# Kernel optimization log

Measured on AMD Instinct MI355X. Metric: run time of the kernel, lower is better.

## Reference

```python
import jax, jax.numpy as jnp
import numpy as np

B, Q, C, N_PER, GS = 8, 2048, 256, 64, 8
H1, H2 = 256, 64
EPS = 1e-5


def make_grid():
    a = jnp.linspace(-0.1, 0.1, GS)
    gx, gy = jnp.meshgrid(a, a, indexing='ij')  # torch.meshgrid default 'ij'
    return jnp.stack([gx.reshape(-1), gy.reshape(-1)], axis=1)  # (n, 2)


def setup_inputs() -> dict:
    key = jax.random.key(0)
    ks = jax.random.split(key, 10)
    s = lambda k, shp, fan: jax.random.normal(k, shp, jnp.float32) / np.sqrt(fan)
    return {
        'tokens': jax.random.normal(ks[0], (B, Q, C), jnp.float32),
        'grid': make_grid(),
        'Wc': s(ks[1], (C, 3), C), 'bc': jnp.zeros((3,), jnp.float32),
        'W1': s(ks[2], (C + 2, H1), C + 2), 'b1': jnp.zeros((H1,), jnp.float32),
        'gamma1': jnp.ones((H1,), jnp.float32), 'beta1': jnp.zeros((H1,), jnp.float32),
        'W2': s(ks[3], (H1, H2), H1), 'b2': jnp.zeros((H2,), jnp.float32),
        'gamma2': jnp.ones((H2,), jnp.float32), 'beta2': jnp.zeros((H2,), jnp.float32),
        'W3': s(ks[4], (H2, 3), H2), 'b3': jnp.zeros((3,), jnp.float32),
    }


def batchnorm(x, gamma, beta):
    # BatchNorm1d in training mode: stats over batch (B*Q) and length (n) dims,
    # per channel (last axis here).
    mean = jnp.mean(x, axis=(0, 1, 2), keepdims=True)
    var = jnp.var(x, axis=(0, 1, 2), keepdims=True)
    return gamma * (x - mean) * jax.lax.rsqrt(var + EPS) + beta


def reference(tokens, grid, Wc, bc, W1, b1, gamma1, beta1, W2, b2, gamma2, beta2, W3, b3):
    coarse = tokens @ Wc + bc  # (B, Q, 3)
    # conv1 (1x1) on concat([tokens_expanded, grid]) == split matmul + broadcast add;
    # avoids materializing the (B,Q,n,C+2) concat explicitly.
    tok_part = tokens @ W1[:C]                 # (B, Q, H1)
    grid_part = grid @ W1[C:]                  # (n, H1)
    h = tok_part[:, :, None, :] + grid_part[None, None, :, :] + b1  # (B, Q, n, H1)
    h = jax.nn.relu(batchnorm(h, gamma1, beta1))
    h = jnp.einsum('bqnc,cd->bqnd', h, W2) + b2  # (B, Q, n, H2)
    h = jax.nn.relu(batchnorm(h, gamma2, beta2))
    disp = jnp.einsum('bqnc,cd->bqnd', h, W3) + b3  # (B, Q, n, 3)
    fine = (coarse[:, :, None, :] + disp).reshape(B, Q * N_PER, 3)
    return coarse, fine
```

## Files before the change

kernel.cpp:

```cpp
#include <hip/hip_runtime.h>
#include <hip/hip_bf16.h>

#define ROWS 16384
#define C_   256
#define H1_  256
#define H2_  64
#define EPSN 1e-5f

typedef __bf16 bf16x8 __attribute__((ext_vector_type(8)));
typedef __bf16 bf16x4 __attribute__((ext_vector_type(4)));
typedef __bf16 bf16x2 __attribute__((ext_vector_type(2)));
typedef float  f32x4  __attribute__((ext_vector_type(4)));
typedef float  f32x2  __attribute__((ext_vector_type(2)));

__device__ __forceinline__ bf16x2 cvt2(float a, float b) {
#if __has_builtin(__builtin_amdgcn_cvt_pk_bf16_f32)
    return __builtin_bit_cast(bf16x2, __builtin_amdgcn_cvt_pk_bf16_f32(a, b));
#else
    bf16x2 r; r[0] = (__bf16)a; r[1] = (__bf16)b; return r;
#endif
}

__global__ __launch_bounds__(256) void k0_pack(const float* __restrict__ W1,
                                               const float* __restrict__ W2,
                                               const float* __restrict__ W3,
                                               __bf16* __restrict__ W1p,
                                               __bf16* __restrict__ W2p,
                                               __bf16* __restrict__ W3p,
                                               float* __restrict__ zero_base) {
    int idx = blockIdx.x * 256 + threadIdx.x;
    if (idx < 65536) {
        int j = idx & 7, l = (idx >> 3) & 63, rest = idx >> 9;
        int ks = rest & 7, CT = rest >> 3;
        int k = ks * 32 + ((l >> 4) << 3) + j;
        int c = CT * 16 + (l & 15);
        W1p[idx] = (__bf16)W1[k * H1_ + c];
    } else {
        int i2 = idx - 65536;
        int j = i2 & 7, l = (i2 >> 3) & 63, rest = i2 >> 9;
        int ks = rest & 7, CK = rest >> 3;
        int k = ks * 32 + ((l >> 4) << 3) + j;
        int c2 = CK * 16 + (l & 15);
        W2p[i2] = (__bf16)W2[k * H2_ + c2];
    }
    if (idx < 1024) {
        int j = idx & 7, l = (idx >> 3) & 63, ks = idx >> 9;
        int k = ks * 32 + ((l >> 4) << 3) + j;
        int c = l & 15;
        W3p[idx] = (c < 3) ? (__bf16)W3[k * 3 + c] : (__bf16)0.f;
    }
    if (idx < 24576) zero_base[idx] = 0.0f;
}

__device__ __forceinline__ void prep_ctx(const float* __restrict__ grid,
                                         const float* __restrict__ W1,
                                         const float* __restrict__ a1p, int c0,
                                         f32x2* wgx2, f32x2* wgy2, float* A_) {
#pragma unroll
    for (int j = 0; j < 8; ++j) A_[j] = grid[2 * j + 1];
    f32x4 a0 = *(const f32x4*)(a1p + c0), a1h = *(const f32x4*)(a1p + c0 + 4);
    f32x4 x0 = *(const f32x4*)(W1 + C_ * H1_ + c0), x1 = *(const f32x4*)(W1 + C_ * H1_ + c0 + 4);
    f32x4 y0 = *(const f32x4*)(W1 + (C_ + 1) * H1_ + c0), yh = *(const f32x4*)(W1 + (C_ + 1) * H1_ + c0 + 4);
    float av[8] = {a0[0], a0[1], a0[2], a0[3], a1h[0], a1h[1], a1h[2], a1h[3]};
    float wx[8] = {x0[0], x0[1], x0[2], x0[3], x1[0], x1[1], x1[2], x1[3]};
    float wy[8] = {y0[0], y0[1], y0[2], y0[3], yh[0], yh[1], yh[2], yh[3]};
#pragma unroll
    for (int e = 0; e < 4; ++e) {
        wgx2[e][0] = av[2 * e] * wx[2 * e];     wgx2[e][1] = av[2 * e + 1] * wx[2 * e + 1];
        wgy2[e][0] = av[2 * e] * wy[2 * e];     wgy2[e][1] = av[2 * e + 1] * wy[2 * e + 1];
    }
}

__device__ __forceinline__ void stage16(__bf16* __restrict__ y1, int w, int c0, int nh,
                                        const float* __restrict__ a1p,
                                        const float* __restrict__ d1p,
                                        const f32x2* wgx2, const f32x2* wgy2,
                                        const float* A_, f32x4 t0, f32x4 t1) {
    f32x4 a0 = *(const f32x4*)(a1p + c0), a1h = *(const f32x4*)(a1p + c0 + 4);
    f32x4 d0 = *(const f32x4*)(d1p + c0), d1h = *(const f32x4*)(d1p + c0 + 4);
    int chunk = c0 >> 3;
    f32x2 base2[4];
    base2[0][0] = fmaf(a0[0], t0[0], d0[0]);  base2[0][1] = fmaf(a0[1], t0[1], d0[1]);
    base2[1][0] = fmaf(a0[2], t0[2], d0[2]);  base2[1][1] = fmaf(a0[3], t0[3], d0[3]);
    base2[2][0] = fmaf(a1h[0], t1[0], d1h[0]); base2[2][1] = fmaf(a1h[1], t1[1], d1h[1]);
    base2[3][0] = fmaf(a1h[2], t1[2], d1h[2]); base2[3][1] = fmaf(a1h[3], t1[3], d1h[3]);
#pragma unroll
    for (int ih = 0; ih < 2; ++ih) {
        float axs = A_[2 * w + ih];
        f32x2 ax2 = {axs, axs};
        f32x2 tc2[4];
#pragma unroll
        for (int e = 0; e < 4; ++e) tc2[e] = __builtin_elementwise_fma(wgx2[e], ax2, base2[e]);
#pragma unroll
        for (int kk = 0; kk < 4; ++kk) {
            int iy = nh + 2 * kk;
            float ays = A_[iy];
            f32x2 ay2 = {ays, ays};
            f32x2 z = {0.f, 0.f};
            int n = w * 16 + ih * 8 + iy;
            bf16x8 out;
            bf16x2* o2 = (bf16x2*)&out;
#pragma unroll
            for (int e = 0; e < 4; ++e) {
                f32x2 v = __builtin_elementwise_max(
                    __builtin_elementwise_fma(wgy2[e], ay2, tc2[e]), z);
                o2[e] = cvt2(v[0], v[1]);
            }
            *(bf16x8*)(&y1[n * 256 + ((chunk ^ iy) << 3)]) = out;
        }
    }
}

__global__ __launch_bounds__(256) void k1a(const float* __restrict__ tokens,
                                           const __bf16* __restrict__ W1p,
                                           const float* __restrict__ Wc,
                                           const float* __restrict__ bc,
                                           float* __restrict__ tokpart,
                                           float* __restrict__ coarse,
                                           float* __restrict__ p1s,
                                           float* __restrict__ p1q) {
    __shared__ __align__(16) __bf16 Al[16 * 264];
    int t = threadIdx.x, w = t >> 6, l = t & 63;
    int quad = l >> 4, col = l & 15;
    int rowbase = (blockIdx.x >> 1) * 16;
    int colhalf = blockIdx.x & 1;
    int slot = blockIdx.x & 31;

    bf16x8 bfr[16];
#pragma unroll
    for (int ctl = 0; ctl < 2; ++ctl)
#pragma unroll
        for (int ks = 0; ks < 8; ++ks) {
            int CT = colhalf * 8 + w * 2 + ctl;
            bfr[ctl * 8 + ks] = *(const bf16x8*)(W1p + (((CT * 8 + ks) * 64 + l) * 8));
        }
    {
        int r = t >> 4, cb = (t & 15) * 16;
        const float* src = tokens + (size_t)(rowbase + r) * C_ + cb;
        f32x4 t0 = *(const f32x4*)(src);
        f32x4 t1 = *(const f32x4*)(src + 4);
        f32x4 t2 = *(const f32x4*)(src + 8);
        f32x4 t3 = *(const f32x4*)(src + 12);
        bf16x8 v0, v1;
        bf16x2* p0 = (bf16x2*)&v0; bf16x2* p1 = (bf16x2*)&v1;
        p0[0] = cvt2(t0[0], t0[1]); p0[1] = cvt2(t0[2], t0[3]);
        p0[2] = cvt2(t1[0], t1[1]); p0[3] = cvt2(t1[2], t1[3]);
        p1[0] = cvt2(t2[0], t2[1]); p1[1] = cvt2(t2[2], t2[3]);
        p1[2] = cvt2(t3[0], t3[1]); p1[3] = cvt2(t3[2], t3[3]);
        *(bf16x8*)(&Al[r * 264 + cb]) = v0;
        *(bf16x8*)(&Al[r * 264 + cb + 8]) = v1;
    }
    __syncthreads();

    bf16x8 af[8];
#pragma unroll
    for (int ks = 0; ks < 8; ++ks)
        af[ks] = *(const bf16x8*)(&Al[col * 264 + ks * 32 + quad * 8]);

#pragma unroll
    for (int ctl = 0; ctl < 2; ++ctl) {
        f32x4 acc = {0.f, 0.f, 0.f, 0.f};
#pragma unroll
        for (int ks = 0; ks < 8; ++ks)
            acc = __builtin_amdgcn_mfma_f32_16x16x32_bf16(af[ks], bfr[ctl * 8 + ks], acc, 0, 0, 0);
        int c = colhalf * 128 + w * 32 + ctl * 16 + col;
        float s = 0.f, q = 0.f;
#pragma unroll
        for (int rr = 0; rr < 4; ++rr) {
            float v = acc[rr];
            tokpart[(size_t)(rowbase + quad * 4 + rr) * C_ + c] = v;
            s += v; q += v * v;
        }
        s += __shfl_xor(s, 16, 64); s += __shfl_xor(s, 32, 64);
        q += __shfl_xor(q, 16, 64); q += __shfl_xor(q, 32, 64);
        if (l < 16) {
            int cc = colhalf * 128 + w * 32 + ctl * 16 + l;
            atomicAdd(p1s + slot * C_ + cc, s);
            atomicAdd(p1q + slot * C_ + cc, q);
        }
    }
    if (colhalf == 0) {
        const f32x4* wcp = (const f32x4*)(Wc + l * 12);
        f32x4 wa = wcp[0], wb = wcp[1], wv = wcp[2];
        float wcl[12] = {wa[0], wa[1], wa[2], wa[3], wb[0], wb[1], wb[2], wb[3],
                         wv[0], wv[1], wv[2], wv[3]};
#pragma unroll
        for (int rr = 0; rr < 4; ++rr) {
            int r = w * 4 + rr;
            bf16x4 tv4 = *(const bf16x4*)(&Al[r * 264 + l * 4]);
            float p[3] = {0.f, 0.f, 0.f};
#pragma unroll
            for (int i = 0; i < 4; ++i) {
                float tvf = (float)tv4[i];
#pragma unroll
                for (int j = 0; j < 3; ++j) p[j] = fmaf(tvf, wcl[i * 3 + j], p[j]);
            }
#pragma unroll
            for (int off = 1; off < 64; off <<= 1)
#pragma unroll
                for (int j = 0; j < 3; ++j) p[j] += __shfl_xor(p[j], off, 64);
            if (l == 0) {
#pragma unroll
                for (int j = 0; j < 3; ++j)
                    coarse[(size_t)(rowbase + r) * 3 + j] = p[j] + bc[j];
            }
        }
    }
}

__global__ void k1b(const float* __restrict__ grid, const float* __restrict__ W1,
                    const float* __restrict__ gamma1, const float* __restrict__ beta1,
                    const float* __restrict__ p1s, const float* __restrict__ p1q,
                    float* __restrict__ a1o, float* __restrict__ d1o) {
    int t = threadIdx.x;
    float S = 0.f, Qq = 0.f;
    for (int s = 0; s < 32; ++s) { S += p1s[s * C_ + t]; Qq += p1q[s * C_ + t]; }
    float mean_t = S / (float)ROWS;
    float var_t = Qq / (float)ROWS - mean_t * mean_t;
    float wx = W1[C_ * H1_ + t];
    float wy = W1[(C_ + 1) * H1_ + t];
    float mg = 0.f, qg = 0.f;
    for (int n = 0; n < 64; ++n) {
        float gv = grid[2 * n] * wx + grid[2 * n + 1] * wy;
        mg += gv; qg += gv * gv;
    }
    mg *= (1.f / 64.f);
    float var_g = qg * (1.f / 64.f) - mg * mg;
    float a1 = gamma1[t] * rsqrtf(var_t + var_g + EPSN);
    a1o[t] = a1;
    d1o[t] = beta1[t] - a1 * (mean_t + mg);
}

template <bool SPILL>
__global__ __launch_bounds__(256) void k2(const float* __restrict__ tokpart,
                                          const float* __restrict__ grid,
                                          const float* __restrict__ W1,
                                          const __bf16* __restrict__ W2p,
                                          const float* __restrict__ a1,
                                          const float* __restrict__ d1,
                                          float* __restrict__ p2s,
                                          float* __restrict__ p2q,
                                          __bf16* __restrict__ h2s) {
    __shared__ __align__(16) __bf16 y1[64 * 256];
    int t = threadIdx.x, w = t >> 6, l = t & 63;
    int quad = l >> 4, col = l & 15;
    int wn = w >> 1, wc = w & 1;
    int c0 = (l & 31) * 8, nh = l >> 5;
    int sw = col & 7;

    bf16x8 bfr[16];
#pragma unroll
    for (int ck = 0; ck < 2; ++ck)
#pragma unroll
        for (int ks = 0; ks < 8; ++ks)
            bfr[ck * 8 + ks] = *(const bf16x8*)(W2p + ((((wc * 2 + ck) * 8 + ks) * 64 + l) * 8));

    f32x2 wgx2[4], wgy2[4]; float A_[8];
    prep_ctx(grid, W1, a1, c0, wgx2, wgy2, A_);

    float s[2][4] = {}, q[2][4] = {};

    const float* tokbase = tokpart + (size_t)blockIdx.x * 8 * C_;
    f32x4 t0 = *(const f32x4*)(tokbase + c0);
    f32x4 t1 = *(const f32x4*)(tokbase + c0 + 4);

#pragma unroll 1
    for (int r8 = 0; r8 < 8; ++r8) {
        int row = blockIdx.x * 8 + r8;
        int nr = (r8 < 7) ? (r8 + 1) : 7;
        f32x4 n0 = *(const f32x4*)(tokbase + (size_t)nr * C_ + c0);
        f32x4 n1 = *(const f32x4*)(tokbase + (size_t)nr * C_ + c0 + 4);

        stage16(y1, w, c0, nh, a1, d1, wgx2, wgy2, A_, t0, t1);
        __syncthreads();
#pragma unroll
        for (int rt = 0; rt < 2; ++rt) {
            int rowb = (wn * 32 + rt * 16 + col) * 256;
            bf16x8 af[8];
#pragma unroll
            for (int ks = 0; ks < 8; ++ks)
                af[ks] = *(const bf16x8*)(&y1[rowb + (((ks * 4 + quad) ^ sw) << 3)]);
#pragma unroll
            for (int ck = 0; ck < 2; ++ck) {
                f32x4 acc = {0.f, 0.f, 0.f, 0.f};
#pragma unroll
                for (int ks = 0; ks < 8; ++ks)
                    acc = __builtin_amdgcn_mfma_f32_16x16x32_bf16(bfr[ck * 8 + ks], af[ks], acc, 0, 0, 0);
#pragma unroll
                for (int rr = 0; rr < 4; ++rr) {
                    s[ck][rr] += acc[rr];
                    q[ck][rr] += acc[rr] * acc[rr];
                }
                if constexpr (SPILL) {
                    bf16x4 v; bf16x2* v2 = (bf16x2*)&v;
                    v2[0] = cvt2(acc[0], acc[1]);
                    v2[1] = cvt2(acc[2], acc[3]);
                    *(bf16x4*)(h2s + (size_t)row * 4096 +
                               ((w * 2 + rt) * 2 + ck) * 256 + l * 4) = v;
                }
            }
        }
        __syncthreads();
        t0 = n0; t1 = n1;
    }
    int slot = ((blockIdx.x << 1) | wn) & 63;
#pragma unroll
    for (int ck = 0; ck < 2; ++ck)
#pragma unroll
        for (int rr = 0; rr < 4; ++rr) {
            float sv = s[ck][rr], qv = q[ck][rr];
            sv += __shfl_xor(sv, 1, 64); sv += __shfl_xor(sv, 2, 64);
            sv += __shfl_xor(sv, 4, 64); sv += __shfl_xor(sv, 8, 64);
            qv += __shfl_xor(qv, 1, 64); qv += __shfl_xor(qv, 2, 64);
            qv += __shfl_xor(qv, 4, 64); qv += __shfl_xor(qv, 8, 64);
            if (col == 0) {
                int c2 = wc * 32 + ck * 16 + quad * 4 + rr;
                atomicAdd(p2s + slot * H2_ + c2, sv);
                atomicAdd(p2q + slot * H2_ + c2, qv);
            }
        }
}

__global__ void k2b(const float* __restrict__ p2s, const float* __restrict__ p2q,
                    const float* __restrict__ gamma2, const float* __restrict__ beta2,
                    float* __restrict__ a2o, float* __restrict__ d2o) {
    int t = threadIdx.x;
    float S = 0.f, Qq = 0.f;
    for (int s = 0; s < 64; ++s) { S += p2s[s * H2_ + t]; Qq += p2q[s * H2_ + t]; }
    const float invN = 1.f / ((float)ROWS * 64.f);
    float mean = S * invN;
    float var = Qq * invN - mean * mean;
    float a2 = gamma2[t] * rsqrtf(var + EPSN);
    a2o[t] = a2;
    d2o[t] = beta2[t] - a2 * mean;
}

__global__ __launch_bounds__(256) void k3s(const __bf16* __restrict__ h2s,
                                           const float* __restrict__ a2,
                                           const float* __restrict__ d2p,
                                           const __bf16* __restrict__ W3p,
                                           const float* __restrict__ b3,
                                           const float* __restrict__ coarse,
                                           float* __restrict__ fine) {
    __shared__ __align__(16) __bf16 y2l[8][64 * 64];
    __shared__ __align__(16) float finebuf[8 * 192];
    int t = threadIdx.x, w = t >> 6, l = t & 63;
    int quad = l >> 4, col = l & 15;
    int wn = w >> 1, wc = w & 1;
    int sw = col & 7;

    bf16x8 wfr[2];
#pragma unroll
    for (int ks = 0; ks < 2; ++ks)
        wfr[ks] = *(const bf16x8*)(W3p + ((ks * 64 + l) * 8));

    float a2v[8], d2v[8];
#pragma unroll
    for (int ck = 0; ck < 2; ++ck)
#pragma unroll
        for (int rr = 0; rr < 4; ++rr) {
            int c2 = wc * 32 + ck * 16 + quad * 4 + rr;
            a2v[ck * 4 + rr] = a2[c2];
            d2v[ck * 4 + rr] = d2p[c2];
        }

#pragma unroll 1
    for (int r8 = 0; r8 < 8; ++r8) {
        size_t row = (size_t)blockIdx.x * 8 + r8;
        const __bf16* src = h2s + row * 4096 + l * 4;
        bf16x4 u[2][2];
#pragma unroll
        for (int rt = 0; rt < 2; ++rt)
#pragma unroll
            for (int ck = 0; ck < 2; ++ck)
                u[rt][ck] = *(const bf16x4*)(src + ((w * 2 + rt) * 2 + ck) * 256);
#pragma unroll
        for (int rt = 0; rt < 2; ++rt) {
            int n = wn * 32 + rt * 16 + col;
#pragma unroll
            for (int ck = 0; ck < 2; ++ck) {
                float y0 = fmaxf(fmaf(a2v[ck * 4 + 0], (float)u[rt][ck][0], d2v[ck * 4 + 0]), 0.f);
                float y1v = fmaxf(fmaf(a2v[ck * 4 + 1], (float)u[rt][ck][1], d2v[ck * 4 + 1]), 0.f);
                float y2 = fmaxf(fmaf(a2v[ck * 4 + 2], (float)u[rt][ck][2], d2v[ck * 4 + 2]), 0.f);
                float y3 = fmaxf(fmaf(a2v[ck * 4 + 3], (float)u[rt][ck][3], d2v[ck * 4 + 3]), 0.f);
                bf16x4 v; bf16x2* v2 = (bf16x2*)&v;
                v2[0] = cvt2(y0, y1v); v2[1] = cvt2(y2, y3);
                int chunk = wc * 4 + ck * 2 + (quad >> 1);
                *(bf16x4*)(&y2l[r8][n * 64 + ((chunk ^ sw) << 3) + (quad & 1) * 4]) = v;
            }
        }
    }
    __syncthreads();
    float b3v = (col < 3) ? b3[col] : 0.f;
#pragma unroll 1
    for (int r8 = 0; r8 < 8; ++r8) {
        int row = blockIdx.x * 8 + r8;
        int rowb = (w * 16 + col) * 64;
        bf16x8 af2[2];
#pragma unroll
        for (int ks = 0; ks < 2; ++ks)
            af2[ks] = *(const bf16x8*)(&y2l[r8][rowb + (((ks * 4 + quad) ^ sw) << 3)]);
        f32x4 acc = {0.f, 0.f, 0.f, 0.f};
        acc = __builtin_amdgcn_mfma_f32_16x16x32_bf16(af2[0], wfr[0], acc, 0, 0, 0);
        acc = __builtin_amdgcn_mfma_f32_16x16x32_bf16(af2[1], wfr[1], acc, 0, 0, 0);
        if (col < 3) {
            float cj = coarse[row * 3 + col] + b3v;
#pragma unroll
            for (int rr = 0; rr < 4; ++rr)
                finebuf[r8 * 192 + (w * 16 + quad * 4 + rr) * 3 + col] = acc[rr] + cj;
        }
    }
    __syncthreads();
    {
        float* dst = fine + (size_t)blockIdx.x * 1536;
        const f32x4* fb = (const f32x4*)finebuf;
        *(f32x4*)(dst + 4 * t) = fb[t];
        if (t < 128) *(f32x4*)(dst + 1024 + 4 * t) = fb[256 + t];
    }
}

__global__ __launch_bounds__(256) void k3r(const float* __restrict__ tokpart,
                                           const float* __restrict__ grid,
                                           const float* __restrict__ W1,
                                           const __bf16* __restrict__ W2p,
                                           const float* __restrict__ a1,
                                           const float* __restrict__ d1,
                                           const __bf16* __restrict__ W3p,
                                           const float* __restrict__ a2,
                                           const float* __restrict__ d2p,
                                           const float* __restrict__ b3,
                                           const float* __restrict__ coarse,
                                           float* __restrict__ fine) {
    __shared__ __align__(16) __bf16 y1[64 * 256];
    __shared__ __align__(16) __bf16 y2l[64 * 72];
    __shared__ __align__(16) float finebuf[8 * 192];
    int t = threadIdx.x, w = t >> 6, l = t & 63;
    int quad = l >> 4, col = l & 15;
    int wn = w >> 1, wc = w & 1;
    int c0 = (l & 31) * 8, nh = l >> 5;
    int sw = col & 7;

    bf16x8 bfr[16];
#pragma unroll
    for (int ck = 0; ck < 2; ++ck)
#pragma unroll
        for (int ks = 0; ks < 8; ++ks)
            bfr[ck * 8 + ks] = *(const bf16x8*)(W2p + ((((wc * 2 + ck) * 8 + ks) * 64 + l) * 8));
    bf16x8 wfr[2];
#pragma unroll
    for (int ks = 0; ks < 2; ++ks)
        wfr[ks] = *(const bf16x8*)(W3p + ((ks * 64 + l) * 8));

    f32x2 wgx2[4], wgy2[4]; float A_[8];
    prep_ctx(grid, W1, a1, c0, wgx2, wgy2, A_);

    float a2v[8], d2v[8];
#pragma unroll
    for (int ck = 0; ck < 2; ++ck)
#pragma unroll
        for (int rr = 0; rr < 4; ++rr) {
            int c2 = wc * 32 + ck * 16 + quad * 4 + rr;
            a2v[ck * 4 + rr] = a2[c2];
            d2v[ck * 4 + rr] = d2p[c2];
        }
    float b3v = (col < 3) ? b3[col] : 0.f;

#pragma unroll 1
    for (int r8 = 0; r8 < 8; ++r8) {
        int row = blockIdx.x * 8 + r8;
        const float* tokrow = tokpart + (size_t)row * C_;
        f32x4 t0 = *(const f32x4*)(tokrow + c0);
        f32x4 t1 = *(const f32x4*)(tokrow + c0 + 4);
        stage16(y1, w, c0, nh, a1, d1, wgx2, wgy2, A_, t0, t1);
        __syncthreads();
#pragma unroll
        for (int rt = 0; rt < 2; ++rt) {
            int rowb = (wn * 32 + rt * 16 + col) * 256;
            bf16x8 af[8];
#pragma unroll
            for (int ks = 0; ks < 8; ++ks)
                af[ks] = *(const bf16x8*)(&y1[rowb + (((ks * 4 + quad) ^ sw) << 3)]);
#pragma unroll
            for (int ck = 0; ck < 2; ++ck) {
                f32x4 acc = {0.f, 0.f, 0.f, 0.f};
#pragma unroll
                for (int ks = 0; ks < 8; ++ks)
                    acc = __builtin_amdgcn_mfma_f32_16x16x32_bf16(bfr[ck * 8 + ks], af[ks], acc, 0, 0, 0);
                bf16x4 v; bf16x2* v2 = (bf16x2*)&v;
                float y0 = fmaxf(fmaf(a2v[ck * 4 + 0], acc[0], d2v[ck * 4 + 0]), 0.f);
                float y1v = fmaxf(fmaf(a2v[ck * 4 + 1], acc[1], d2v[ck * 4 + 1]), 0.f);
                float y2 = fmaxf(fmaf(a2v[ck * 4 + 2], acc[2], d2v[ck * 4 + 2]), 0.f);
                float y3 = fmaxf(fmaf(a2v[ck * 4 + 3], acc[3], d2v[ck * 4 + 3]), 0.f);
                v2[0] = cvt2(y0, y1v); v2[1] = cvt2(y2, y3);
                *(bf16x4*)(&y2l[(wn * 32 + rt * 16 + col) * 72 + wc * 32 + ck * 16 + quad * 4]) = v;
            }
        }
        __syncthreads();
        bf16x8 af2[2];
#pragma unroll
        for (int ks = 0; ks < 2; ++ks)
            af2[ks] = *(const bf16x8*)(&y2l[(w * 16 + col) * 72 + ks * 32 + quad * 8]);
        f32x4 d2acc = {0.f, 0.f, 0.f, 0.f};
        d2acc = __builtin_amdgcn_mfma_f32_16x16x32_bf16(af2[0], wfr[0], d2acc, 0, 0, 0);
        d2acc = __builtin_amdgcn_mfma_f32_16x16x32_bf16(af2[1], wfr[1], d2acc, 0, 0, 0);
        if (col < 3) {
            float cj = coarse[row * 3 + col] + b3v;
#pragma unroll
            for (int rr = 0; rr < 4; ++rr)
                finebuf[r8 * 192 + (w * 16 + quad * 4 + rr) * 3 + col] = d2acc[rr] + cj;
        }
        __syncthreads();
    }
    {
        float* dst = fine + (size_t)blockIdx.x * 1536;
        const f32x4* fb = (const f32x4*)finebuf;
        *(f32x4*)(dst + 4 * t) = fb[t];
        if (t < 128) *(f32x4*)(dst + 1024 + 4 * t) = fb[256 + t];
    }
}

extern "C" void kernel_launch(void* const* d_in, const int* in_sizes, int n_in,
                              void* d_out, int out_size, void* d_ws, size_t ws_size,
                              hipStream_t stream) {
    (void)in_sizes; (void)n_in; (void)out_size;
    const float* tokens = (const float*)d_in[0];
    const float* grid   = (const float*)d_in[1];
    const float* Wc     = (const float*)d_in[2];
    const float* bc     = (const float*)d_in[3];
    const float* W1     = (const float*)d_in[4];
    const float* gamma1 = (const float*)d_in[6];
    const float* beta1  = (const float*)d_in[7];
    const float* W2     = (const float*)d_in[8];
    const float* gamma2 = (const float*)d_in[10];
    const float* beta2  = (const float*)d_in[11];
    const float* W3     = (const float*)d_in[12];
    const float* b3     = (const float*)d_in[13];

    char* ws = (char*)d_ws;
    __bf16* W1p     = (__bf16*)(ws);
    __bf16* W2p     = (__bf16*)(ws + 131072);
    float*  p1s     = (float*)(ws + 163840);
    float*  p1q     = (float*)(ws + 196608);
    float*  p2s     = (float*)(ws + 229376);
    float*  p2q     = (float*)(ws + 245760);
    float*  a1      = (float*)(ws + 262144);
    float*  d1      = (float*)(ws + 263168);
    float*  a2      = (float*)(ws + 264192);
    float*  d2p     = (float*)(ws + 264448);
    __bf16* W3p     = (__bf16*)(ws + 264704);
    float*  tokpart = (float*)(ws + 266752);
    __bf16* h2s     = (__bf16*)(ws + 17043968);

    const size_t SPILL_NEED = 17043968ull + 134217728ull;
    bool spill = ws_size >= SPILL_NEED;

    float* coarse = (float*)d_out;
    float* fine   = (float*)d_out + (size_t)ROWS * 3;

    k0_pack<<<320, 256, 0, stream>>>(W1, W2, W3, W1p, W2p, W3p, p1s);
    k1a<<<2048, 256, 0, stream>>>(tokens, W1p, Wc, bc, tokpart, coarse, p1s, p1q);
    k1b<<<1, 256, 0, stream>>>(grid, W1, gamma1, beta1, p1s, p1q, a1, d1);
    if (spill) {
        k2<true><<<ROWS / 8, 256, 0, stream>>>(tokpart, grid, W1, W2p, a1, d1, p2s, p2q, h2s);
        k2b<<<1, 64, 0, stream>>>(p2s, p2q, gamma2, beta2, a2, d2p);
        k3s<<<ROWS / 8, 256, 0, stream>>>(h2s, a2, d2p, W3p, b3, coarse, fine);
    } else {
        k2<false><<<ROWS / 8, 256, 0, stream>>>(tokpart, grid, W1, W2p, a1, d1, p2s, p2q, h2s);
        k2b<<<1, 64, 0, stream>>>(p2s, p2q, gamma2, beta2, a2, d2p);
        k3r<<<ROWS / 8, 256, 0, stream>>>(tokpart, grid, W1, W2p, a1, d1, W3p, a2, d2p, b3, coarse, fine);
    }
}
```

Before: 203.5 us.

## Make each wave own whole row tiles to drop block barriers in k2 and k3s

In k2, each wave now computes all 64 output channels for its own 16 grid points instead of splitting points and channels across wave pairs. Each wave only reads the LDS rows it staged itself, so both per-iteration __syncthreads are removed. k3s follows the same per-wave ownership with a small wave-private LDS buffer, fusing its load/normalize pass with the MFMA pass and dropping the block barrier between them. The trade-off is twice as many W2 fragments held in registers (launch bounds now request 2 blocks per CU), which raises register pressure, and correctness now depends on stage16 writing only rows its own wave consumes.

```diff
diff --git a/kernel.cpp b/kernel.cpp
--- a/kernel.cpp
+++ b/kernel.cpp
@@ -232,33 +232,32 @@
 }
 
 template <bool SPILL>
-__global__ __launch_bounds__(256) void k2(const float* __restrict__ tokpart,
-                                          const float* __restrict__ grid,
-                                          const float* __restrict__ W1,
-                                          const __bf16* __restrict__ W2p,
-                                          const float* __restrict__ a1,
-                                          const float* __restrict__ d1,
-                                          float* __restrict__ p2s,
-                                          float* __restrict__ p2q,
-                                          __bf16* __restrict__ h2s) {
+__global__ __launch_bounds__(256, 2) void k2(const float* __restrict__ tokpart,
+                                             const float* __restrict__ grid,
+                                             const float* __restrict__ W1,
+                                             const __bf16* __restrict__ W2p,
+                                             const float* __restrict__ a1,
+                                             const float* __restrict__ d1,
+                                             float* __restrict__ p2s,
+                                             float* __restrict__ p2q,
+                                             __bf16* __restrict__ h2s) {
     __shared__ __align__(16) __bf16 y1[64 * 256];
     int t = threadIdx.x, w = t >> 6, l = t & 63;
     int quad = l >> 4, col = l & 15;
-    int wn = w >> 1, wc = w & 1;
     int c0 = (l & 31) * 8, nh = l >> 5;
     int sw = col & 7;
 
-    bf16x8 bfr[16];
-#pragma unroll
-    for (int ck = 0; ck < 2; ++ck)
+    bf16x8 bfr[32];
+#pragma unroll
+    for (int ck = 0; ck < 4; ++ck)
 #pragma unroll
         for (int ks = 0; ks < 8; ++ks)
-            bfr[ck * 8 + ks] = *(const bf16x8*)(W2p + ((((wc * 2 + ck) * 8 + ks) * 64 + l) * 8));
+            bfr[ck * 8 + ks] = *(const bf16x8*)(W2p + (((ck * 8 + ks) * 64 + l) * 8));
 
     f32x2 wgx2[4], wgy2[4]; float A_[8];
     prep_ctx(grid, W1, a1, c0, wgx2, wgy2, A_);
 
-    float s[2][4] = {}, q[2][4] = {};
+    float s[4][4] = {}, q[4][4] = {};
 
     const float* tokbase = tokpart + (size_t)blockIdx.x * 8 * C_;
     f32x4 t0 = *(const f32x4*)(tokbase + c0);
@@ -272,40 +271,34 @@
         f32x4 n1 = *(const f32x4*)(tokbase + (size_t)nr * C_ + c0 + 4);
 
         stage16(y1, w, c0, nh, a1, d1, wgx2, wgy2, A_, t0, t1);
-        __syncthreads();
-#pragma unroll
-        for (int rt = 0; rt < 2; ++rt) {
-            int rowb = (wn * 32 + rt * 16 + col) * 256;
-            bf16x8 af[8];
+        int rowb = (w * 16 + col) * 256;
+        bf16x8 af[8];
+#pragma unroll
+        for (int ks = 0; ks < 8; ++ks)
+            af[ks] = *(const bf16x8*)(&y1[rowb + (((ks * 4 + quad) ^ sw) << 3)]);
+#pragma unroll
+        for (int ck = 0; ck < 4; ++ck) {
+            f32x4 acc = {0.f, 0.f, 0.f, 0.f};
 #pragma unroll
             for (int ks = 0; ks < 8; ++ks)
-                af[ks] = *(const bf16x8*)(&y1[rowb + (((ks * 4 + quad) ^ sw) << 3)]);
-#pragma unroll
-            for (int ck = 0; ck < 2; ++ck) {
-                f32x4 acc = {0.f, 0.f, 0.f, 0.f};
-#pragma unroll
-                for (int ks = 0; ks < 8; ++ks)
-                    acc = __builtin_amdgcn_mfma_f32_16x16x32_bf16(bfr[ck * 8 + ks], af[ks], acc, 0, 0, 0);
-#pragma unroll
-                for (int rr = 0; rr < 4; ++rr) {
-                    s[ck][rr] += acc[rr];
-                    q[ck][rr] += acc[rr] * acc[rr];
-                }
-                if constexpr (SPILL) {
-                    bf16x4 v; bf16x2* v2 = (bf16x2*)&v;
-                    v2[0] = cvt2(acc[0], acc[1]);
-                    v2[1] = cvt2(acc[2], acc[3]);
-                    *(bf16x4*)(h2s + (size_t)row * 4096 +
-                               ((w * 2 + rt) * 2 + ck) * 256 + l * 4) = v;
-                }
-            }
-        }
-        __syncthreads();
+                acc = __builtin_amdgcn_mfma_f32_16x16x32_bf16(bfr[ck * 8 + ks], af[ks], acc, 0, 0, 0);
+#pragma unroll
+            for (int rr = 0; rr < 4; ++rr) {
+                s[ck][rr] += acc[rr];
+                q[ck][rr] += acc[rr] * acc[rr];
+            }
+            if constexpr (SPILL) {
+                bf16x4 v; bf16x2* v2 = (bf16x2*)&v;
+                v2[0] = cvt2(acc[0], acc[1]);
+                v2[1] = cvt2(acc[2], acc[3]);
+                *(bf16x4*)(h2s + (size_t)row * 4096 + (w * 4 + ck) * 256 + l * 4) = v;
+            }
+        }
         t0 = n0; t1 = n1;
     }
-    int slot = ((blockIdx.x << 1) | wn) & 63;
-#pragma unroll
-    for (int ck = 0; ck < 2; ++ck)
+    int slot = ((blockIdx.x << 2) | w) & 63;
+#pragma unroll
+    for (int ck = 0; ck < 4; ++ck)
 #pragma unroll
         for (int rr = 0; rr < 4; ++rr) {
             float sv = s[ck][rr], qv = q[ck][rr];
@@ -314,7 +307,7 @@
             qv += __shfl_xor(qv, 1, 64); qv += __shfl_xor(qv, 2, 64);
             qv += __shfl_xor(qv, 4, 64); qv += __shfl_xor(qv, 8, 64);
             if (col == 0) {
-                int c2 = wc * 32 + ck * 16 + quad * 4 + rr;
+                int c2 = ck * 16 + quad * 4 + rr;
                 atomicAdd(p2s + slot * H2_ + c2, sv);
                 atomicAdd(p2q + slot * H2_ + c2, qv);
             }
@@ -342,11 +335,10 @@
                                            const float* __restrict__ b3,
                                            const float* __restrict__ coarse,
                                            float* __restrict__ fine) {
-    __shared__ __align__(16) __bf16 y2l[8][64 * 64];
+    __shared__ __align__(16) __bf16 y2l[4][16 * 64];
     __shared__ __align__(16) float finebuf[8 * 192];
     int t = threadIdx.x, w = t >> 6, l = t & 63;
     int quad = l >> 4, col = l & 15;
-    int wn = w >> 1, wc = w & 1;
     int sw = col & 7;
 
     bf16x8 wfr[2];
@@ -354,52 +346,41 @@
     for (int ks = 0; ks < 2; ++ks)
         wfr[ks] = *(const bf16x8*)(W3p + ((ks * 64 + l) * 8));
 
-    float a2v[8], d2v[8];
-#pragma unroll
-    for (int ck = 0; ck < 2; ++ck)
+    float a2v[16], d2v[16];
+#pragma unroll
+    for (int ck = 0; ck < 4; ++ck)
 #pragma unroll
         for (int rr = 0; rr < 4; ++rr) {
-            int c2 = wc * 32 + ck * 16 + quad * 4 + rr;
+            int c2 = ck * 16 + quad * 4 + rr;
             a2v[ck * 4 + rr] = a2[c2];
             d2v[ck * 4 + rr] = d2p[c2];
         }
-
-#pragma unroll 1
-    for (int r8 = 0; r8 < 8; ++r8) {
-        size_t row = (size_t)blockIdx.x * 8 + r8;
-        const __bf16* src = h2s + row * 4096 + l * 4;
-        bf16x4 u[2][2];
-#pragma unroll
-        for (int rt = 0; rt < 2; ++rt)
-#pragma unroll
-            for (int ck = 0; ck < 2; ++ck)
-                u[rt][ck] = *(const bf16x4*)(src + ((w * 2 + rt) * 2 + ck) * 256);
-#pragma unroll
-        for (int rt = 0; rt < 2; ++rt) {
-            int n = wn * 32 + rt * 16 + col;
-#pragma unroll
-            for (int ck = 0; ck < 2; ++ck) {
-                float y0 = fmaxf(fmaf(a2v[ck * 4 + 0], (float)u[rt][ck][0], d2v[ck * 4 + 0]), 0.f);
-                float y1v = fmaxf(fmaf(a2v[ck * 4 + 1], (float)u[rt][ck][1], d2v[ck * 4 + 1]), 0.f);
-                float y2 = fmaxf(fmaf(a2v[ck * 4 + 2], (float)u[rt][ck][2], d2v[ck * 4 + 2]), 0.f);
-                float y3 = fmaxf(fmaf(a2v[ck * 4 + 3], (float)u[rt][ck][3], d2v[ck * 4 + 3]), 0.f);
-                bf16x4 v; bf16x2* v2 = (bf16x2*)&v;
-                v2[0] = cvt2(y0, y1v); v2[1] = cvt2(y2, y3);
-                int chunk = wc * 4 + ck * 2 + (quad >> 1);
-                *(bf16x4*)(&y2l[r8][n * 64 + ((chunk ^ sw) << 3) + (quad & 1) * 4]) = v;
-            }
-        }
-    }
-    __syncthreads();
     float b3v = (col < 3) ? b3[col] : 0.f;
+    __bf16* yw = &y2l[w][0];
+
 #pragma unroll 1
     for (int r8 = 0; r8 < 8; ++r8) {
         int row = blockIdx.x * 8 + r8;
-        int rowb = (w * 16 + col) * 64;
+        const __bf16* src = h2s + (size_t)row * 4096 + l * 4;
+        bf16x4 u[4];
+#pragma unroll
+        for (int ck = 0; ck < 4; ++ck)
+            u[ck] = *(const bf16x4*)(src + (w * 4 + ck) * 256);
+#pragma unroll
+        for (int ck = 0; ck < 4; ++ck) {
+            float y0 = fmaxf(fmaf(a2v[ck * 4 + 0], (float)u[ck][0], d2v[ck * 4 + 0]), 0.f);
+            float y1v = fmaxf(fmaf(a2v[ck * 4 + 1], (float)u[ck][1], d2v[ck * 4 + 1]), 0.f);
+            float y2 = fmaxf(fmaf(a2v[ck * 4 + 2], (float)u[ck][2], d2v[ck * 4 + 2]), 0.f);
+            float y3 = fmaxf(fmaf(a2v[ck * 4 + 3], (float)u[ck][3], d2v[ck * 4 + 3]), 0.f);
+            bf16x4 v; bf16x2* v2 = (bf16x2*)&v;
+            v2[0] = cvt2(y0, y1v); v2[1] = cvt2(y2, y3);
+            int chunk = ck * 2 + (quad >> 1);
+            *(bf16x4*)(&yw[col * 64 + ((chunk ^ sw) << 3) + (quad & 1) * 4]) = v;
+        }
         bf16x8 af2[2];
 #pragma unroll
         for (int ks = 0; ks < 2; ++ks)
-            af2[ks] = *(const bf16x8*)(&y2l[r8][rowb + (((ks * 4 + quad) ^ sw) << 3)]);
+            af2[ks] = *(const bf16x8*)(&yw[col * 64 + (((ks * 4 + quad) ^ sw) << 3)]);
         f32x4 acc = {0.f, 0.f, 0.f, 0.f};
         acc = __builtin_amdgcn_mfma_f32_16x16x32_bf16(af2[0], wfr[0], acc, 0, 0, 0);
         acc = __builtin_amdgcn_mfma_f32_16x16x32_bf16(af2[1], wfr[1], acc, 0, 0, 0);
```

Result: no change. 203.7 us (+0.1%).
